# Kernel optimization log

Measured on AMD Instinct MI355X. Metric: run time of the kernel, lower is better.

The kernel has to match this reference:

```python
import jax, jax.numpy as jnp
import numpy as np

N = 100000
E = 1600000
D = 128      # input feature dim
H = 128      # hidden_channels
O = 2        # out_channels
NEG_SLOPE = 0.2
EPS = 1e-16  # PyG softmax denominator epsilon


def gat_conv(x, src, dst, W_src, W_dst, att_src, att_dst, bias):
    """PyG GATConv, heads=1, add_self_loops=False, concat=True."""
    xs = x @ W_src                      # [N, C]
    xd = x @ W_dst                      # [N, C]
    a_s = xs @ att_src                  # [N]
    a_d = xd @ att_dst                  # [N]
    e = jax.nn.leaky_relu(a_s[src] + a_d[dst], NEG_SLOPE)   # [E]
    # segment softmax over edges grouped by destination node
    m = jax.ops.segment_max(e, dst, num_segments=N)          # [N]
    m = jnp.where(jnp.isfinite(m), m, 0.0)
    ex = jnp.exp(e - m[dst])                                  # [E]
    denom = jax.ops.segment_sum(ex, dst, num_segments=N)      # [N]
    alpha = ex / (denom[dst] + EPS)                            # [E]
    msg = alpha[:, None] * xs[src]                             # [E, C]
    out = jax.ops.segment_sum(msg, dst, num_segments=N)       # [N, C]
    return out + bias


def setup_inputs() -> dict:
    key = jax.random.key(0)
    ks = jax.random.split(key, 14)
    s = lambda k, shape, fan: jax.random.normal(k, shape, jnp.float32) * (1.0 / np.sqrt(fan))
    x = jax.random.normal(ks[0], (N, D), jnp.float32)
    edge_index = jax.random.randint(ks[1], (2, E), 0, N, dtype=jnp.int32)
    return {
        "x": x,
        "edge_index": edge_index,
        "W1s": s(ks[2], (D, H), D), "W1d": s(ks[3], (D, H), D),
        "a1s": s(ks[4], (H,), H),   "a1d": s(ks[5], (H,), H),
        "b1": jnp.zeros((H,), jnp.float32),
        "W2s": s(ks[6], (H, H), H), "W2d": s(ks[7], (H, H), H),
        "a2s": s(ks[8], (H,), H),   "a2d": s(ks[9], (H,), H),
        "b2": jnp.zeros((H,), jnp.float32),
        "Wl": s(ks[10], (H, O), H), "bl": jnp.zeros((O,), jnp.float32),
    }


def reference(x, edge_index, W1s, W1d, a1s, a1d, b1, W2s, W2d, a2s, a2d, b2, Wl, bl):
    src, dst = edge_index[0], edge_index[1]
    h = jax.nn.relu(gat_conv(x, src, dst, W1s, W1d, a1s, a1d, b1))
    # dropout p=0.3 is identity at inference
    h = jax.nn.relu(gat_conv(h, src, dst, W2s, W2d, a2s, a2d, b2))
    return h @ Wl + bl  # [N, O]
```

## Files before the change

### kernel.cpp

```cpp
#include <hip/hip_runtime.h>
#include <hip/hip_fp16.h>

#define NBSHIFT 9
#define BSZ     512
#define CAP     12288

typedef _Float16 f16x8 __attribute__((ext_vector_type(8)));
typedef float    f32x4 __attribute__((ext_vector_type(4)));

__global__ void k_init(int* __restrict__ cursor, int nb,
                       const float* __restrict__ W1d, const float* __restrict__ a1d,
                       const float* __restrict__ W2d, const float* __restrict__ a2d,
                       float* __restrict__ vv,
                       const float* __restrict__ W1s, const float* __restrict__ W2s,
                       _Float16* __restrict__ Wh1, _Float16* __restrict__ Wh2) {
    int b = blockIdx.x, t = threadIdx.x;
    if (b == 0) {
        if (t < nb) cursor[t] = 0;
    } else if (b <= 2) {
        if (t < 128) {
            const float* W = (b == 1) ? W1d : W2d;
            const float* a = (b == 1) ? a1d : a2d;
            float s = 0.f;
            for (int j = 0; j < 128; j++) s += W[t * 128 + j] * a[j];
            vv[(b - 1) * 128 + t] = s;
        }
    } else {
        const float* W = (b == 3) ? W1s : W2s;
        _Float16* Wh = (b == 3) ? Wh1 : Wh2;
        int n = t & 127, k0 = (t >> 7) * 64;
        _Float16 buf[64];
#pragma unroll
        for (int j = 0; j < 64; j++) buf[j] = (_Float16)W[(k0 + j) * 128 + n];
        uint4* dp = (uint4*)&Wh[n * 128 + k0];
        const uint4* sp = (const uint4*)buf;
#pragma unroll
        for (int i = 0; i < 8; i++) dp[i] = sp[i];
    }
}


__device__ __forceinline__ void gemm_mfma_body(
        const float* __restrict__ X, const _Float16* __restrict__ Wh,
        const float* __restrict__ att, const float* __restrict__ vd,
        __half* __restrict__ Y, float* __restrict__ a_s, float* __restrict__ a_d,
        int N, int blk) {
    int t = threadIdx.x;
    int l = t & 63, wv = t >> 6;
    int quad = l >> 4, lm = l & 15;
    int rbase = blk * 64 + wv * 16;
    int arow = rbase + lm;
    bool rok = arow < N;
    const float* xrow = X + (size_t)arow * 128;

    f32x4 acc[8];
#pragma unroll
    for (int c = 0; c < 8; c++) acc[c] = (f32x4){0.f, 0.f, 0.f, 0.f};
    float adp = 0.f;

#pragma unroll
    for (int kc = 0; kc < 4; kc++) {
        int k0 = kc * 32 + quad * 8;
        float xf[8];
        if (rok) {
            *(float4*)&xf[0] = *(const float4*)&xrow[k0];
            *(float4*)&xf[4] = *(const float4*)&xrow[k0 + 4];
        } else {
#pragma unroll
            for (int j = 0; j < 8; j++) xf[j] = 0.f;
        }
        float4 v0 = *(const float4*)&vd[k0];
        float4 v1 = *(const float4*)&vd[k0 + 4];
        adp += xf[0] * v0.x + xf[1] * v0.y + xf[2] * v0.z + xf[3] * v0.w
             + xf[4] * v1.x + xf[5] * v1.y + xf[6] * v1.z + xf[7] * v1.w;
        f16x8 af;
#pragma unroll
        for (int j = 0; j < 8; j++) af[j] = (_Float16)xf[j];
        const _Float16* wb = Wh + (size_t)lm * 128 + k0;
#pragma unroll
        for (int c = 0; c < 8; c++) {
            f16x8 bf = *(const f16x8*)(wb + c * 2048);
            acc[c] = __builtin_amdgcn_mfma_f32_16x16x32_f16(af, bf, acc[c], 0, 0, 0);
        }
    }

    adp += __shfl_xor(adp, 16);
    adp += __shfl_xor(adp, 32);
    if (quad == 0 && rok) a_d[arow] = adp;

    float attc[8];
#pragma unroll
    for (int c = 0; c < 8; c++) attc[c] = att[c * 16 + lm];
#pragma unroll
    for (int r = 0; r < 4; r++) {
        int grow = rbase + quad * 4 + r;
        bool gok = grow < N;
        float p = 0.f;
#pragma unroll
        for (int c = 0; c < 8; c++) {
            if (gok) Y[(size_t)grow * 128 + c * 16 + lm] = __float2half(acc[c][r]);
            p += acc[c][r] * attc[c];
        }
        p += __shfl_xor(p, 1); p += __shfl_xor(p, 2); p += __shfl_xor(p, 4); p += __shfl_xor(p, 8);
        if (lm == 0 && gok) a_s[grow] = p;
    }
}

__global__ __launch_bounds__(256, 4) void k_fuse1(
        const float* __restrict__ X, const _Float16* __restrict__ Wh,
        const float* __restrict__ att, const float* __restrict__ vd,
        __half* __restrict__ Y, float* __restrict__ a_s, float* __restrict__ a_d, int N, int gb,
        const int* __restrict__ src, const int* __restrict__ dst, int E,
        int* __restrict__ cursor, unsigned* __restrict__ pairs) {
    __shared__ int sh[512];
    int t = threadIdx.x;

    if ((int)blockIdx.x >= gb) {
        int* hist  = sh;
        int* start = sh + 256;
        hist[t] = 0;
        __syncthreads();
        int e0 = (blockIdx.x - gb) * 1024 + t * 4;
        int d[4], s[4];
        bool full = (e0 + 3 < E);
        if (full) {
            int4 dv = *(const int4*)&dst[e0];
            int4 sv = *(const int4*)&src[e0];
            d[0] = dv.x; d[1] = dv.y; d[2] = dv.z; d[3] = dv.w;
            s[0] = sv.x; s[1] = sv.y; s[2] = sv.z; s[3] = sv.w;
#pragma unroll
            for (int i = 0; i < 4; i++) atomicAdd(&hist[d[i] >> NBSHIFT], 1);
        } else {
#pragma unroll
            for (int i = 0; i < 4; i++) {
                if (e0 + i < E) { d[i] = dst[e0 + i]; s[i] = src[e0 + i]; atomicAdd(&hist[d[i] >> NBSHIFT], 1); }
                else d[i] = -1;
            }
        }
        __syncthreads();
        if (hist[t] > 0) start[t] = atomicAdd(&cursor[t], hist[t]);
        __syncthreads();
        hist[t] = 0;
        __syncthreads();
#pragma unroll
        for (int i = 0; i < 4; i++) {
            if (full || (e0 + i < E)) {
                int b = d[i] >> NBSHIFT;
                int r = atomicAdd(&hist[b], 1);
                pairs[b * CAP + start[b] + r] = ((unsigned)(d[i] & (BSZ - 1)) << 17) | (unsigned)s[i];
            }
        }
        return;
    }

    gemm_mfma_body(X, Wh, att, vd, Y, a_s, a_d, N, blockIdx.x);
}

__global__ __launch_bounds__(256, 4) void k_gemm2(
        const float* __restrict__ X, const _Float16* __restrict__ Wh,
        const float* __restrict__ att, const float* __restrict__ vd,
        __half* __restrict__ Y, float* __restrict__ a_s, float* __restrict__ a_d, int N) {
    gemm_mfma_body(X, Wh, att, vd, Y, a_s, a_d, N, blockIdx.x);
}

__global__ __launch_bounds__(256) void kB_csr(const unsigned* __restrict__ pairs,
                                              const int* __restrict__ cursor,
                                              int* __restrict__ row_start, int* __restrict__ row_end,
                                              int* __restrict__ csr_src, int N) {
    __shared__ int cnt[BSZ];
    __shared__ int cur[BSZ];
    __shared__ int sS[256];
    int b = blockIdx.x, t = threadIdx.x;
    int base = b * CAP;
    int ecnt = cursor[b];
    int nodeBase = b << NBSHIFT;
    cnt[t] = 0; cnt[t + 256] = 0;
    __syncthreads();
    for (int j = t; j < ecnt; j += 256)
        atomicAdd(&cnt[pairs[base + j] >> 17], 1);
    __syncthreads();
    int c0 = cnt[t * 2], c1 = cnt[t * 2 + 1];
    int run = c0 + c1;
    sS[t] = run; __syncthreads();
    for (int off = 1; off < 256; off <<= 1) {
        int x = (t >= off) ? sS[t - off] : 0;
        __syncthreads();
        sS[t] += x;
        __syncthreads();
    }
    int exb = sS[t] - run;
    {
        int li0 = t * 2, li1 = t * 2 + 1;
        int g0 = nodeBase + li0, g1 = nodeBase + li1;
        cur[li0] = exb;
        cur[li1] = exb + c0;
        if (g0 < N) { row_start[g0] = base + exb;      row_end[g0] = base + exb + c0; }
        if (g1 < N) { row_start[g1] = base + exb + c0; row_end[g1] = base + exb + c0 + c1; }
    }
    __syncthreads();
    for (int j = t; j < ecnt; j += 256) {
        unsigned p = pairs[base + j];
        int r = atomicAdd(&cur[p >> 17], 1);
        csr_src[base + r] = (int)(p & 0x1FFFFu);
    }
}

template <bool HEAD>
__global__ __launch_bounds__(256) void k_agg(const int* __restrict__ csr_src, const int* __restrict__ row_start,
                                             const int* __restrict__ row_end,
                                             const float* __restrict__ a_s, const float* __restrict__ a_d,
                                             const __half* __restrict__ xs, const float* __restrict__ bias,
                                             const float* __restrict__ Wl, const float* __restrict__ bl,
                                             float* __restrict__ out, int N) {
    int t = threadIdx.x; int wv = t >> 6, l = t & 63;
    int n = blockIdx.x * 4 + wv;
    if (n >= N) return;
    int rs = row_start[n], re = row_end[n];
    int deg = re - rs;
    float adn = a_d[n];
    int q = l >> 4;
    int c = (l & 15) * 8;

    float aA[8], aB[8];
#pragma unroll
    for (int k = 0; k < 8; k++) { aA[k] = 0.f; aB[k] = 0.f; }
    float dn = 0.f;
    const int* cs = csr_src + rs;

    int i = q;
    for (; i + 4 < deg; i += 8) {
        int sA = cs[i];
        int sB = cs[i + 4];
        float tA = a_s[sA] + adn;
        float tB = a_s[sB] + adn;
        tA = tA > 0.f ? tA : 0.2f * tA;
        tB = tB > 0.f ? tB : 0.2f * tB;
        float exA = __expf(tA);
        float exB = __expf(tB);
        dn += exA + exB;
        uint4 uA = *(const uint4*)&xs[(size_t)sA * 128 + c];
        uint4 uB = *(const uint4*)&xs[(size_t)sB * 128 + c];
        const __half2* hA = (const __half2*)&uA;
        const __half2* hB = (const __half2*)&uB;
#pragma unroll
        for (int k = 0; k < 4; k++) {
            float2 fA = __half22float2(hA[k]);
            float2 fB = __half22float2(hB[k]);
            aA[2 * k] += exA * fA.x; aA[2 * k + 1] += exA * fA.y;
            aB[2 * k] += exB * fB.x; aB[2 * k + 1] += exB * fB.y;
        }
    }
    for (; i < deg; i += 4) {
        int s = cs[i];
        float tv = a_s[s] + adn;
        tv = tv > 0.f ? tv : 0.2f * tv;
        float ex = __expf(tv);
        dn += ex;
        uint4 u = *(const uint4*)&xs[(size_t)s * 128 + c];
        const __half2* h2 = (const __half2*)&u;
#pragma unroll
        for (int k = 0; k < 4; k++) {
            float2 f = __half22float2(h2[k]);
            aA[2 * k] += ex * f.x; aA[2 * k + 1] += ex * f.y;
        }
    }

    dn += __shfl_xor(dn, 16);
    dn += __shfl_xor(dn, 32);
    float inv = 1.f / (dn + 1e-16f);

    float hv[8];
    float4 b0 = *(const float4*)&bias[c];
    float4 b1 = *(const float4*)&bias[c + 4];
    float bb[8] = {b0.x, b0.y, b0.z, b0.w, b1.x, b1.y, b1.z, b1.w};
#pragma unroll
    for (int k = 0; k < 8; k++) {
        float v = aA[k] + aB[k];
        v += __shfl_xor(v, 16);
        v += __shfl_xor(v, 32);
        v = v * inv + bb[k];
        hv[k] = v > 0.f ? v : 0.f;
    }

    if (HEAD) {
        float p0 = 0.f, p1 = 0.f;
#pragma unroll
        for (int k = 0; k < 8; k++) {
            p0 += hv[k] * Wl[2 * (c + k)];
            p1 += hv[k] * Wl[2 * (c + k) + 1];
        }
#pragma unroll
        for (int o = 8; o > 0; o >>= 1) { p0 += __shfl_xor(p0, o); p1 += __shfl_xor(p1, o); }
        if (l == 0) { out[2 * n] = p0 + bl[0]; out[2 * n + 1] = p1 + bl[1]; }
    } else {
        if (q == 0) {
            *(float4*)&out[(size_t)n * 128 + c]     = make_float4(hv[0], hv[1], hv[2], hv[3]);
            *(float4*)&out[(size_t)n * 128 + c + 4] = make_float4(hv[4], hv[5], hv[6], hv[7]);
        }
    }
}


extern "C" void kernel_launch(void* const* d_in, const int* in_sizes, int n_in,
                              void* d_out, int out_size, void* d_ws, size_t ws_size,
                              hipStream_t stream) {
    const float* x   = (const float*)d_in[0];
    const int*   ei  = (const int*)d_in[1];
    const float* W1s = (const float*)d_in[2];
    const float* W1d = (const float*)d_in[3];
    const float* a1s = (const float*)d_in[4];
    const float* a1d = (const float*)d_in[5];
    const float* b1  = (const float*)d_in[6];
    const float* W2s = (const float*)d_in[7];
    const float* W2d = (const float*)d_in[8];
    const float* a2s = (const float*)d_in[9];
    const float* a2d = (const float*)d_in[10];
    const float* b2  = (const float*)d_in[11];
    const float* Wl  = (const float*)d_in[12];
    const float* bl  = (const float*)d_in[13];
    float* out = (float*)d_out;

    int N = in_sizes[0] / 128;
    int E = in_sizes[1] / 2;
    const int* srcA = ei;
    const int* dstA = ei + E;
    int NB = (N + BSZ - 1) >> NBSHIFT;

    __half* xs = (__half*)d_ws;
    float* h   = (float*)(xs + (size_t)N * 128);
    float* as_ = h + (size_t)N * 128;
    float* ad_ = as_ + N;
    float* vv  = ad_ + N;
    int* row_start = (int*)(vv + 256);
    int* row_end   = row_start + N;
    int* csr_src   = row_end + N;
    int* cursor    = csr_src + (size_t)NB * CAP;
    _Float16* Wh1  = (_Float16*)(cursor + 256);
    _Float16* Wh2  = Wh1 + 16384;
    unsigned* pairs = (unsigned*)h;

    int gb = (N + 63) / 64;
    int EB = (E + 1023) / 1024;
    int ab = (N + 3) / 4;

    k_init<<<5, 256, 0, stream>>>(cursor, NB, W1d, a1d, W2d, a2d, vv, W1s, W2s, Wh1, Wh2);

    k_fuse1<<<gb + EB, 256, 0, stream>>>(x, Wh1, a1s, vv, xs, as_, ad_, N, gb,
                                         srcA, dstA, E, cursor, pairs);

    kB_csr<<<NB, 256, 0, stream>>>(pairs, cursor, row_start, row_end, csr_src, N);

    k_agg<false><<<ab, 256, 0, stream>>>(csr_src, row_start, row_end, as_, ad_, xs, b1, nullptr, nullptr, h, N);

    k_gemm2<<<gb, 256, 0, stream>>>(h, Wh2, a2s, vv + 128, xs, as_, ad_, N);

    k_agg<true><<<ab, 256, 0, stream>>>(csr_src, row_start, row_end, as_, ad_, xs, b2, Wl, bl, out, N);
}
```

Measured before the change: 364.1 us.

## Drop weight-prep kernel, stage weights per block in LDS, use 256-node buckets

Removes the k_init kernel: each GEMM block now converts W_src to fp16 into shared memory and computes the W_dst·att vector itself, and the cursor is cleared with hipMemsetAsync. Bucket size drops from 512 to 256 nodes, so there are twice as many CSR buckets and the scatter histogram grows to 512 entries. The intent is to cut one launch and its serialization and to read weights from LDS instead of global memory. The cost is redundant per-block weight conversion (over 1500 blocks each reading 64KB), more LDS per block which may reduce occupancy, and more buckets contending on the cursor atomics.

```diff
diff --git a/kernel.cpp b/kernel.cpp
--- a/kernel.cpp
+++ b/kernel.cpp
@@ -1,51 +1,50 @@
 #include <hip/hip_runtime.h>
 #include <hip/hip_fp16.h>
 
-#define NBSHIFT 9
-#define BSZ     512
-#define CAP     12288
+#define NBSHIFT 8
+#define BSZ     256
+#define CAP     5120
 
 typedef _Float16 f16x8 __attribute__((ext_vector_type(8)));
 typedef float    f32x4 __attribute__((ext_vector_type(4)));
 
-__global__ void k_init(int* __restrict__ cursor, int nb,
-                       const float* __restrict__ W1d, const float* __restrict__ a1d,
-                       const float* __restrict__ W2d, const float* __restrict__ a2d,
-                       float* __restrict__ vv,
-                       const float* __restrict__ W1s, const float* __restrict__ W2s,
-                       _Float16* __restrict__ Wh1, _Float16* __restrict__ Wh2) {
-    int b = blockIdx.x, t = threadIdx.x;
-    if (b == 0) {
-        if (t < nb) cursor[t] = 0;
-    } else if (b <= 2) {
-        if (t < 128) {
-            const float* W = (b == 1) ? W1d : W2d;
-            const float* a = (b == 1) ? a1d : a2d;
-            float s = 0.f;
-            for (int j = 0; j < 128; j++) s += W[t * 128 + j] * a[j];
-            vv[(b - 1) * 128 + t] = s;
-        }
-    } else {
-        const float* W = (b == 3) ? W1s : W2s;
-        _Float16* Wh = (b == 3) ? Wh1 : Wh2;
-        int n = t & 127, k0 = (t >> 7) * 64;
-        _Float16 buf[64];
-#pragma unroll
-        for (int j = 0; j < 64; j++) buf[j] = (_Float16)W[(k0 + j) * 128 + n];
-        uint4* dp = (uint4*)&Wh[n * 128 + k0];
-        const uint4* sp = (const uint4*)buf;
-#pragma unroll
-        for (int i = 0; i < 8; i++) dp[i] = sp[i];
-    }
-}
-
-
-__device__ __forceinline__ void gemm_mfma_body(
-        const float* __restrict__ X, const _Float16* __restrict__ Wh,
-        const float* __restrict__ att, const float* __restrict__ vd,
+
+#define GEMM_LDS_BYTES (128 * 136 * 2 + 512)
+
+__device__ __forceinline__ void gemm_body(
+        const float* __restrict__ X, const float* __restrict__ Ws,
+        const float* __restrict__ Wd, const float* __restrict__ attd,
+        const float* __restrict__ att,
         __half* __restrict__ Y, float* __restrict__ a_s, float* __restrict__ a_d,
-        int N, int blk) {
+        int N, int blk, char* smem) {
+    _Float16 (*sWh)[136] = (_Float16(*)[136])smem;
+    float* svd = (float*)(smem + 128 * 136 * 2);
     int t = threadIdx.x;
+
+    if (t < 128) {
+        const float4* wr = (const float4*)&Wd[t * 128];
+        const float4* ar = (const float4*)attd;
+        float s = 0.f;
+#pragma unroll 8
+        for (int j = 0; j < 32; j++) {
+            float4 w = wr[j], a = ar[j];
+            s += w.x * a.x + w.y * a.y + w.z * a.z + w.w * a.w;
+        }
+        svd[t] = s;
+    }
+#pragma unroll
+    for (int i = 0; i < 16; i++) {
+        int gid = t + i * 256;
+        int n = gid & 127, kq = gid >> 7;
+        _Float16 p[4];
+        p[0] = (_Float16)Ws[(kq * 4 + 0) * 128 + n];
+        p[1] = (_Float16)Ws[(kq * 4 + 1) * 128 + n];
+        p[2] = (_Float16)Ws[(kq * 4 + 2) * 128 + n];
+        p[3] = (_Float16)Ws[(kq * 4 + 3) * 128 + n];
+        *(uint2*)&sWh[n][kq * 4] = *(uint2*)p;
+    }
+    __syncthreads();
+
     int l = t & 63, wv = t >> 6;
     int quad = l >> 4, lm = l & 15;
     int rbase = blk * 64 + wv * 16;
@@ -69,17 +68,16 @@
 #pragma unroll
             for (int j = 0; j < 8; j++) xf[j] = 0.f;
         }
-        float4 v0 = *(const float4*)&vd[k0];
-        float4 v1 = *(const float4*)&vd[k0 + 4];
+        float4 v0 = *(const float4*)&svd[k0];
+        float4 v1 = *(const float4*)&svd[k0 + 4];
         adp += xf[0] * v0.x + xf[1] * v0.y + xf[2] * v0.z + xf[3] * v0.w
              + xf[4] * v1.x + xf[5] * v1.y + xf[6] * v1.z + xf[7] * v1.w;
         f16x8 af;
 #pragma unroll
         for (int j = 0; j < 8; j++) af[j] = (_Float16)xf[j];
-        const _Float16* wb = Wh + (size_t)lm * 128 + k0;
 #pragma unroll
         for (int c = 0; c < 8; c++) {
-            f16x8 bf = *(const f16x8*)(wb + c * 2048);
+            f16x8 bf = *(const f16x8*)&sWh[c * 16 + lm][k0];
             acc[c] = __builtin_amdgcn_mfma_f32_16x16x32_f16(af, bf, acc[c], 0, 0, 0);
         }
     }
@@ -107,18 +105,19 @@
 }
 
 __global__ __launch_bounds__(256, 4) void k_fuse1(
-        const float* __restrict__ X, const _Float16* __restrict__ Wh,
-        const float* __restrict__ att, const float* __restrict__ vd,
+        const float* __restrict__ X, const float* __restrict__ W1s,
+        const float* __restrict__ W1d, const float* __restrict__ a1d,
+        const float* __restrict__ a1s,
         __half* __restrict__ Y, float* __restrict__ a_s, float* __restrict__ a_d, int N, int gb,
         const int* __restrict__ src, const int* __restrict__ dst, int E,
         int* __restrict__ cursor, unsigned* __restrict__ pairs) {
-    __shared__ int sh[512];
+    __shared__ __align__(16) char smem[GEMM_LDS_BYTES];
     int t = threadIdx.x;
 
     if ((int)blockIdx.x >= gb) {
-        int* hist  = sh;
-        int* start = sh + 256;
-        hist[t] = 0;
+        int* hist  = (int*)smem;
+        int* start = hist + 512;
+        hist[t] = 0; hist[t + 256] = 0;
         __syncthreads();
         int e0 = (blockIdx.x - gb) * 1024 + t * 4;
         int d[4], s[4];
@@ -138,9 +137,10 @@
             }
         }
         __syncthreads();
-        if (hist[t] > 0) start[t] = atomicAdd(&cursor[t], hist[t]);
-        __syncthreads();
-        hist[t] = 0;
+        if (hist[t] > 0)       start[t]       = atomicAdd(&cursor[t],       hist[t]);
+        if (hist[t + 256] > 0) start[t + 256] = atomicAdd(&cursor[t + 256], hist[t + 256]);
+        __syncthreads();
+        hist[t] = 0; hist[t + 256] = 0;
         __syncthreads();
 #pragma unroll
         for (int i = 0; i < 4; i++) {
@@ -153,14 +153,16 @@
         return;
     }
 
-    gemm_mfma_body(X, Wh, att, vd, Y, a_s, a_d, N, blockIdx.x);
+    gemm_body(X, W1s, W1d, a1d, a1s, Y, a_s, a_d, N, blockIdx.x, smem);
 }
 
 __global__ __launch_bounds__(256, 4) void k_gemm2(
-        const float* __restrict__ X, const _Float16* __restrict__ Wh,
-        const float* __restrict__ att, const float* __restrict__ vd,
+        const float* __restrict__ X, const float* __restrict__ W2s,
+        const float* __restrict__ W2d, const float* __restrict__ a2d,
+        const float* __restrict__ a2s,
         __half* __restrict__ Y, float* __restrict__ a_s, float* __restrict__ a_d, int N) {
-    gemm_mfma_body(X, Wh, att, vd, Y, a_s, a_d, N, blockIdx.x);
+    __shared__ __align__(16) char smem[GEMM_LDS_BYTES];
+    gemm_body(X, W2s, W2d, a2d, a2s, Y, a_s, a_d, N, blockIdx.x, smem);
 }
 
 __global__ __launch_bounds__(256) void kB_csr(const unsigned* __restrict__ pairs,
@@ -174,29 +176,23 @@
     int base = b * CAP;
     int ecnt = cursor[b];
     int nodeBase = b << NBSHIFT;
-    cnt[t] = 0; cnt[t + 256] = 0;
+    cnt[t] = 0;
     __syncthreads();
     for (int j = t; j < ecnt; j += 256)
         atomicAdd(&cnt[pairs[base + j] >> 17], 1);
     __syncthreads();
-    int c0 = cnt[t * 2], c1 = cnt[t * 2 + 1];
-    int run = c0 + c1;
-    sS[t] = run; __syncthreads();
+    int c0 = cnt[t];
+    sS[t] = c0; __syncthreads();
     for (int off = 1; off < 256; off <<= 1) {
         int x = (t >= off) ? sS[t - off] : 0;
         __syncthreads();
         sS[t] += x;
         __syncthreads();
     }
-    int exb = sS[t] - run;
-    {
-        int li0 = t * 2, li1 = t * 2 + 1;
-        int g0 = nodeBase + li0, g1 = nodeBase + li1;
-        cur[li0] = exb;
-        cur[li1] = exb + c0;
-        if (g0 < N) { row_start[g0] = base + exb;      row_end[g0] = base + exb + c0; }
-        if (g1 < N) { row_start[g1] = base + exb + c0; row_end[g1] = base + exb + c0 + c1; }
-    }
+    int excl = sS[t] - c0;
+    cur[t] = excl;
+    int g = nodeBase + t;
+    if (g < N) { row_start[g] = base + excl; row_end[g] = base + excl + c0; }
     __syncthreads();
     for (int j = t; j < ecnt; j += 256) {
         unsigned p = pairs[base + j];
@@ -204,6 +200,7 @@
         csr_src[base + r] = (int)(p & 0x1FFFFu);
     }
 }
+
 
 template <bool HEAD>
 __global__ __launch_bounds__(256) void k_agg(const int* __restrict__ csr_src, const int* __restrict__ row_start,
@@ -330,29 +327,26 @@
     float* h   = (float*)(xs + (size_t)N * 128);
     float* as_ = h + (size_t)N * 128;
     float* ad_ = as_ + N;
-    float* vv  = ad_ + N;
-    int* row_start = (int*)(vv + 256);
+    int* row_start = (int*)(ad_ + N);
     int* row_end   = row_start + N;
     int* csr_src   = row_end + N;
     int* cursor    = csr_src + (size_t)NB * CAP;
-    _Float16* Wh1  = (_Float16*)(cursor + 256);
-    _Float16* Wh2  = Wh1 + 16384;
     unsigned* pairs = (unsigned*)h;
 
     int gb = (N + 63) / 64;
     int EB = (E + 1023) / 1024;
     int ab = (N + 3) / 4;
 
-    k_init<<<5, 256, 0, stream>>>(cursor, NB, W1d, a1d, W2d, a2d, vv, W1s, W2s, Wh1, Wh2);
-
-    k_fuse1<<<gb + EB, 256, 0, stream>>>(x, Wh1, a1s, vv, xs, as_, ad_, N, gb,
+    hipMemsetAsync(cursor, 0, (size_t)NB * 4, stream);
+
+    k_fuse1<<<gb + EB, 256, 0, stream>>>(x, W1s, W1d, a1d, a1s, xs, as_, ad_, N, gb,
                                          srcA, dstA, E, cursor, pairs);
 
     kB_csr<<<NB, 256, 0, stream>>>(pairs, cursor, row_start, row_end, csr_src, N);
 
     k_agg<false><<<ab, 256, 0, stream>>>(csr_src, row_start, row_end, as_, ad_, xs, b1, nullptr, nullptr, h, N);
 
-    k_gemm2<<<gb, 256, 0, stream>>>(h, Wh2, a2s, vv + 128, xs, as_, ad_, N);
+    k_gemm2<<<gb, 256, 0, stream>>>(h, W2s, W2d, a2d, a2s, xs, as_, ad_, N);
 
     k_agg<true><<<ab, 256, 0, stream>>>(csr_src, row_start, row_end, as_, ad_, xs, b2, Wl, bl, out, N);
 }
```

After: 337.1 us. 7.4% less time.
